# Kernel tuning notes

Measured on AMD Instinct MI355X. Metric: run time of the kernel, lower is better.

The kernel has to match this reference:

```python
import jax, jax.numpy as jnp
import numpy as np
from jax.ops import segment_sum, segment_max

N, E, F_IN, H1, H2, HEADS, OUT, G = 50000, 800000, 64, 64, 64, 4, 32, 500

def setup_inputs() -> dict:
    key = jax.random.key(0)
    ks = jax.random.split(key, 12)
    x = jax.random.normal(ks[0], (N, F_IN), dtype=jnp.float32)
    edge_index = jax.random.randint(ks[1], (2, E), 0, N, dtype=jnp.int64)
    batch = jnp.sort(jax.random.randint(ks[2], (N,), 0, G, dtype=jnp.int64))
    def glorot(k, shape):
        fan = shape[0] + shape[-1]
        return jax.random.uniform(k, shape, jnp.float32, -1.0, 1.0) * jnp.sqrt(6.0 / fan)
    return {
        "x": x,
        "edge_index": edge_index,
        "batch": batch,
        "gcn_W": glorot(ks[3], (F_IN, H1)),
        "gcn_b": jnp.zeros((H1,), jnp.float32),
        "gat_W": glorot(ks[4], (H1, HEADS * H2)),
        "att_src": glorot(ks[5], (HEADS, H2)),
        "att_dst": glorot(ks[6], (HEADS, H2)),
        "gat_b": jnp.zeros((HEADS * H2,), jnp.float32),
        "out_W": glorot(ks[7], (HEADS * H2, OUT)),
        "out_b": jnp.zeros((OUT,), jnp.float32),
    }

def reference(x, edge_index, batch, gcn_W, gcn_b, gat_W, att_src, att_dst, gat_b, out_W, out_b):
    n = x.shape[0]
    loop = jnp.arange(n)
    # edges with self-loops: src (j) -> dst (i), PyG convention
    src = jnp.concatenate([edge_index[0], loop])
    dst = jnp.concatenate([edge_index[1], loop])

    # ---- GCNConv: symmetric normalized scatter-add ----
    h = x @ gcn_W                                            # [N, H1]
    deg = segment_sum(jnp.ones_like(dst, dtype=h.dtype), dst, num_segments=n)
    dinv = jnp.where(deg > 0, jax.lax.rsqrt(deg), 0.0)       # deg^{-1/2}
    norm = dinv[src] * dinv[dst]                             # [E']
    h = segment_sum(norm[:, None] * h[src], dst, num_segments=n) + gcn_b
    h = jax.nn.relu(h)

    # ---- GATConv: per-edge attention + segment softmax over dst ----
    g = (h @ gat_W).reshape(n, HEADS, H2)                    # [N, H, C]
    a_s = jnp.einsum('nhc,hc->nh', g, att_src)               # [N, H]
    a_d = jnp.einsum('nhc,hc->nh', g, att_dst)
    e = jax.nn.leaky_relu(a_s[src] + a_d[dst], 0.2)          # [E', H]
    m = segment_max(e, dst, num_segments=n)                  # every node has a self-loop
    e = jnp.exp(e - m[dst])
    denom = segment_sum(e, dst, num_segments=n)
    alpha = e / denom[dst]                                   # [E', H]
    agg = segment_sum(alpha[:, :, None] * g[src], dst, num_segments=n)  # [N, H, C]
    z = jax.nn.relu(agg.reshape(n, HEADS * H2) + gat_b)

    # ---- global mean pool over graphs + output linear ----
    cnt = segment_sum(jnp.ones((n,), z.dtype), batch, num_segments=G)
    pooled = segment_sum(z, batch, num_segments=G) / jnp.maximum(cnt, 1.0)[:, None]
    return pooled @ out_W + out_b
```

## Files before the change

### kernel.cpp

```cpp
#include <hip/hip_runtime.h>
#include <math.h>

#define NN 50000
#define NE 800000
#define NEP (NE + NN)
#define NGRAPH 500
#define NOUT 32
#define NBLK 196

typedef _Float16 half4 __attribute__((ext_vector_type(4)));
typedef _Float16 half2v __attribute__((ext_vector_type(2)));

__device__ __forceinline__ float lrelu(float x) { return x > 0.f ? x : 0.2f * x; }
__device__ __forceinline__ half2v bch2(float f) { return __builtin_bit_cast(half2v, f); }

__device__ __forceinline__ unsigned fkey(float f) {
    unsigned b = __float_as_uint(f);
    return (b & 0x80000000u) ? ~b : (b | 0x80000000u);
}
__device__ __forceinline__ float funkey(unsigned k) {
    unsigned b = (k & 0x80000000u) ? (k & 0x7fffffffu) : ~k;
    return __uint_as_float(b);
}


__global__ void k_count(const int* __restrict__ dst, int* __restrict__ cnt,
                        int* __restrict__ pos) {
    int e = blockIdx.x * blockDim.x + threadIdx.x;
    if (e < NE) pos[e] = atomicAdd(&cnt[dst[e]], 1);
}

__global__ __launch_bounds__(256) void k_scan1(const int* __restrict__ cnt, int* __restrict__ bsum,
                                               float* __restrict__ pool, float* __restrict__ cnt_g) {
    __shared__ int buf[256];
    int gid = blockIdx.x * 256 + threadIdx.x;
    int v = (gid < NN) ? (cnt[gid] + 1) : 0;
    buf[threadIdx.x] = v;
    for (int j = gid; j < NGRAPH * 256; j += NBLK * 256) pool[j] = 0.f;
    if (gid < NGRAPH) cnt_g[gid] = 0.f;
    __syncthreads();
    for (int off = 128; off; off >>= 1) {
        if (threadIdx.x < off) buf[threadIdx.x] += buf[threadIdx.x + off];
        __syncthreads();
    }
    if (threadIdx.x == 0) bsum[blockIdx.x] = buf[0];
}

__global__ __launch_bounds__(256) void k_scan3(const int* __restrict__ cnt,
                                               const int* __restrict__ bsum,
                                               int* __restrict__ row_ptr,
                                               float* __restrict__ dinv,
                                               int* __restrict__ col) {
    __shared__ int sb[256];
    __shared__ int buf[256];
    int tid = threadIdx.x;
    int bv = (tid < NBLK) ? bsum[tid] : 0;
    sb[tid] = bv;
    __syncthreads();
    for (int off = 1; off < 256; off <<= 1) {
        int t = (tid >= off) ? sb[tid - off] : 0;
        __syncthreads();
        sb[tid] += t;
        __syncthreads();
    }
    int blockoff = (blockIdx.x == 0) ? 0 : sb[blockIdx.x - 1];
    int i = blockIdx.x * 256 + tid;
    int v = (i < NN) ? (cnt[i] + 1) : 0;
    buf[tid] = v;
    __syncthreads();
    for (int off = 1; off < 256; off <<= 1) {
        int t = (tid >= off) ? buf[tid - off] : 0;
        __syncthreads();
        buf[tid] += t;
        __syncthreads();
    }
    if (i < NN) {
        int rp = blockoff + buf[tid] - v;
        row_ptr[i] = rp;
        dinv[i] = rsqrtf((float)(cnt[i] + 1));
        col[rp] = i;
    }
    if (i == 0) row_ptr[NN] = NEP;
}

__global__ void k_fill(const int* __restrict__ src, const int* __restrict__ dst,
                       const int* __restrict__ row_ptr, const int* __restrict__ pos,
                       int* __restrict__ col) {
    int idx = blockIdx.x * blockDim.x + threadIdx.x;
    if (idx < NE) {
        int d = dst[idx];
        col[row_ptr[d] + 1 + pos[idx]] = src[idx];
    }
}


__global__ __launch_bounds__(256) void k_gemm64(const float* __restrict__ A,
                                                const float* __restrict__ B,
                                                const float* __restrict__ dinv,
                                                _Float16* __restrict__ C16, int n) {
    __shared__ float Bs[64 * 64];
    __shared__ float As[64 * 68];
    int tid = threadIdx.x;
    int rb = blockIdx.x * 64;
    for (int i = tid; i < 1024; i += 256) ((float4*)Bs)[i] = ((const float4*)B)[i];
    for (int i = tid; i < 1024; i += 256) {
        int r = i >> 4, c = i & 15;
        int row = rb + r; if (row >= n) row = n - 1;
        ((float4*)As)[r * 17 + c] = ((const float4*)A)[(size_t)row * 16 + c];
    }
    __syncthreads();
    int lane = tid & 63, wv = tid >> 6;
    int fl = lane & 15, sub = lane >> 4;
    int r0 = wv * 16 + sub * 4;
    const float4* Bs4 = (const float4*)Bs;
    float4 acc0 = {0,0,0,0}, acc1 = {0,0,0,0}, acc2 = {0,0,0,0}, acc3 = {0,0,0,0};
#pragma unroll 4
    for (int k = 0; k < 64; ++k) {
        float4 b4 = Bs4[k * 16 + fl];
        float a0 = As[(r0 + 0) * 68 + k];
        float a1 = As[(r0 + 1) * 68 + k];
        float a2 = As[(r0 + 2) * 68 + k];
        float a3 = As[(r0 + 3) * 68 + k];
        acc0.x += a0 * b4.x; acc0.y += a0 * b4.y; acc0.z += a0 * b4.z; acc0.w += a0 * b4.w;
        acc1.x += a1 * b4.x; acc1.y += a1 * b4.y; acc1.z += a1 * b4.z; acc1.w += a1 * b4.w;
        acc2.x += a2 * b4.x; acc2.y += a2 * b4.y; acc2.z += a2 * b4.z; acc2.w += a2 * b4.w;
        acc3.x += a3 * b4.x; acc3.y += a3 * b4.y; acc3.z += a3 * b4.z; acc3.w += a3 * b4.w;
    }
    int row = rb + r0;
    float d0 = dinv[row + 0 < n ? row + 0 : n - 1];
    float d1 = dinv[row + 1 < n ? row + 1 : n - 1];
    float d2 = dinv[row + 2 < n ? row + 2 : n - 1];
    float d3 = dinv[row + 3 < n ? row + 3 : n - 1];
    half4 h0, h1, h2, h3;
    h0.x=(_Float16)(acc0.x*d0); h0.y=(_Float16)(acc0.y*d0); h0.z=(_Float16)(acc0.z*d0); h0.w=(_Float16)(acc0.w*d0);
    h1.x=(_Float16)(acc1.x*d1); h1.y=(_Float16)(acc1.y*d1); h1.z=(_Float16)(acc1.z*d1); h1.w=(_Float16)(acc1.w*d1);
    h2.x=(_Float16)(acc2.x*d2); h2.y=(_Float16)(acc2.y*d2); h2.z=(_Float16)(acc2.z*d2); h2.w=(_Float16)(acc2.w*d2);
    h3.x=(_Float16)(acc3.x*d3); h3.y=(_Float16)(acc3.y*d3); h3.z=(_Float16)(acc3.z*d3); h3.w=(_Float16)(acc3.w*d3);
    if (row + 0 < n) ((half4*)(C16 + (size_t)(row + 0) * 64))[fl] = h0;
    if (row + 1 < n) ((half4*)(C16 + (size_t)(row + 1) * 64))[fl] = h1;
    if (row + 2 < n) ((half4*)(C16 + (size_t)(row + 2) * 64))[fl] = h2;
    if (row + 3 < n) ((half4*)(C16 + (size_t)(row + 3) * 64))[fl] = h3;
}


__global__ void k_uv(const float* __restrict__ gat_W, const float* __restrict__ att_src,
                     const float* __restrict__ att_dst, float* __restrict__ UV) {
    int idx = blockIdx.x * blockDim.x + threadIdx.x;
    if (idx >= 512) return;
    int f = idx >> 3, o = idx & 7, h = o & 3;
    const float* av = (o < 4) ? att_src : att_dst;
    float s = 0.f;
#pragma unroll 8
    for (int c = 0; c < 64; ++c) s += gat_W[f * 256 + h * 64 + c] * av[h * 64 + c];
    UV[idx] = s;
}


__global__ void k_w16t(const float* __restrict__ W, _Float16* __restrict__ W16T) {
    int idx = blockIdx.x * blockDim.x + threadIdx.x;
    if (idx >= 64 * 256) return;
    int c = idx >> 6, f = idx & 63;
    W16T[idx] = (_Float16)W[f * 256 + c];
}


__global__ __launch_bounds__(256) void k_gcn_agg(const _Float16* __restrict__ hxs16,
                                                 const int* __restrict__ row_ptr,
                                                 const int* __restrict__ col,
                                                 const float* __restrict__ dinv,
                                                 const float* __restrict__ bias,
                                                 const float* __restrict__ UV,
                                                 _Float16* __restrict__ h16,
                                                 float* __restrict__ a_s,
                                                 float* __restrict__ a_d) {
    int wid = (blockIdx.x * blockDim.x + threadIdx.x) >> 6;
    int lane = threadIdx.x & 63;
    if (wid >= NN) return;
    int slot = lane >> 4;
    int fl   = lane & 15;
    int s0 = row_ptr[wid], s1 = row_ptr[wid + 1];
    float di = dinv[wid];
    const half4* hx4 = (const half4*)hxs16;
    float ax = 0.f, ay = 0.f, az = 0.f, aw = 0.f;
    int k = s0 + slot;
    for (; k + 12 < s1; k += 16) {
        int i0 = col[k], i1 = col[k + 4], i2 = col[k + 8], i3 = col[k + 12];
        half4 v0 = hx4[(size_t)i0 * 16 + fl];
        half4 v1 = hx4[(size_t)i1 * 16 + fl];
        half4 v2 = hx4[(size_t)i2 * 16 + fl];
        half4 v3 = hx4[(size_t)i3 * 16 + fl];
        ax += ((float)v0.x + (float)v1.x) + ((float)v2.x + (float)v3.x);
        ay += ((float)v0.y + (float)v1.y) + ((float)v2.y + (float)v3.y);
        az += ((float)v0.z + (float)v1.z) + ((float)v2.z + (float)v3.z);
        aw += ((float)v0.w + (float)v1.w) + ((float)v2.w + (float)v3.w);
    }
    for (; k < s1; k += 4) {
        half4 v = hx4[(size_t)col[k] * 16 + fl];
        ax += (float)v.x; ay += (float)v.y;
        az += (float)v.z; aw += (float)v.w;
    }
    ax += __shfl_xor(ax, 16); ax += __shfl_xor(ax, 32);
    ay += __shfl_xor(ay, 16); ay += __shfl_xor(ay, 32);
    az += __shfl_xor(az, 16); az += __shfl_xor(az, 32);
    aw += __shfl_xor(aw, 16); aw += __shfl_xor(aw, 32);
    float4 bb = ((const float4*)bias)[fl];
    float zx = fmaxf(ax * di + bb.x, 0.f);
    float zy = fmaxf(ay * di + bb.y, 0.f);
    float zz = fmaxf(az * di + bb.z, 0.f);
    float zw = fmaxf(aw * di + bb.w, 0.f);
    if (slot == 0) {
        half4 z;
        z.x = (_Float16)zx; z.y = (_Float16)zy; z.z = (_Float16)zz; z.w = (_Float16)zw;
        ((half4*)(h16 + (size_t)wid * 64))[fl] = z;
    }
    int f0 = fl * 4;
    float ps = zx * UV[(f0 + 0) * 8 + slot] + zy * UV[(f0 + 1) * 8 + slot]
             + zz * UV[(f0 + 2) * 8 + slot] + zw * UV[(f0 + 3) * 8 + slot];
    float pd = zx * UV[(f0 + 0) * 8 + 4 + slot] + zy * UV[(f0 + 1) * 8 + 4 + slot]
             + zz * UV[(f0 + 2) * 8 + 4 + slot] + zw * UV[(f0 + 3) * 8 + 4 + slot];
    ps += __shfl_xor(ps, 1); pd += __shfl_xor(pd, 1);
    ps += __shfl_xor(ps, 2); pd += __shfl_xor(pd, 2);
    ps += __shfl_xor(ps, 4); pd += __shfl_xor(pd, 4);
    ps += __shfl_xor(ps, 8); pd += __shfl_xor(pd, 8);
    if (fl == 0) {
        a_s[wid * 4 + slot] = ps;
        a_d[wid * 4 + slot] = pd;
    }
}


__global__ __launch_bounds__(256) void k_gmax(const float* __restrict__ a_s,
                                              unsigned* __restrict__ gmaxU) {
    __shared__ unsigned sm[4];
    int tid = threadIdx.x;
    if (tid < 4) sm[tid] = 0u;
    __syncthreads();
    float mx = -1e30f, my = -1e30f, mz = -1e30f, mw = -1e30f;
    int stride = gridDim.x * 256;
    for (int n = blockIdx.x * 256 + tid; n < NN; n += stride) {
        float4 v = ((const float4*)a_s)[n];
        mx = fmaxf(mx, v.x); my = fmaxf(my, v.y);
        mz = fmaxf(mz, v.z); mw = fmaxf(mw, v.w);
    }
    atomicMax(&sm[0], fkey(mx)); atomicMax(&sm[1], fkey(my));
    atomicMax(&sm[2], fkey(mz)); atomicMax(&sm[3], fkey(mw));
    __syncthreads();
    if (tid < 4) atomicMax(&gmaxU[tid], sm[tid]);
}


__global__ __launch_bounds__(256) void k_gat_h(const _Float16* __restrict__ h16,
                                               const float* __restrict__ a_s,
                                               const float* __restrict__ a_d,
                                               const int* __restrict__ row_ptr,
                                               const int* __restrict__ col,
                                               const unsigned* __restrict__ gmaxU,
                                               _Float16* __restrict__ aggH) {
    int tid = threadIdx.x;
    int wv = tid >> 6, lane = tid & 63;
    int wid = blockIdx.x * 4 + wv;
    int slot = lane >> 4;
    int fl = lane & 15;

    int s0 = row_ptr[wid], s1 = row_ptr[wid + 1];
    float4 ad4 = ((const float4*)a_d)[wid];
    float M0 = lrelu(funkey(gmaxU[0]) + ad4.x);
    float M1 = lrelu(funkey(gmaxU[1]) + ad4.y);
    float M2 = lrelu(funkey(gmaxU[2]) + ad4.z);
    float M3 = lrelu(funkey(gmaxU[3]) + ad4.w);
    const half4* h4 = (const half4*)h16;
    const float4* as4 = (const float4*)a_s;

    float t0 = 1e-30f, t1 = 1e-30f, t2 = 1e-30f, t3 = 1e-30f;
    float4 A0 = {0,0,0,0}, A1 = {0,0,0,0}, A2 = {0,0,0,0}, A3 = {0,0,0,0};

    int k = s0 + slot;
    for (; k + 4 < s1; k += 8) {
        int ia = col[k], ib = col[k + 4];
        float4 ea = as4[ia];
        float4 eb = as4[ib];
        half4 va = h4[(size_t)ia * 16 + fl];
        half4 vb = h4[(size_t)ib * 16 + fl];
        float wa0 = __expf(lrelu(ea.x + ad4.x) - M0);
        float wa1 = __expf(lrelu(ea.y + ad4.y) - M1);
        float wa2 = __expf(lrelu(ea.z + ad4.z) - M2);
        float wa3 = __expf(lrelu(ea.w + ad4.w) - M3);
        float wb0 = __expf(lrelu(eb.x + ad4.x) - M0);
        float wb1 = __expf(lrelu(eb.y + ad4.y) - M1);
        float wb2 = __expf(lrelu(eb.z + ad4.z) - M2);
        float wb3 = __expf(lrelu(eb.w + ad4.w) - M3);
        t0 += wa0 + wb0; t1 += wa1 + wb1; t2 += wa2 + wb2; t3 += wa3 + wb3;
        float vax = (float)va.x, vay = (float)va.y, vaz = (float)va.z, vaw = (float)va.w;
        float vbx = (float)vb.x, vby = (float)vb.y, vbz = (float)vb.z, vbw = (float)vb.w;
        A0.x += wa0 * vax + wb0 * vbx; A0.y += wa0 * vay + wb0 * vby;
        A0.z += wa0 * vaz + wb0 * vbz; A0.w += wa0 * vaw + wb0 * vbw;
        A1.x += wa1 * vax + wb1 * vbx; A1.y += wa1 * vay + wb1 * vby;
        A1.z += wa1 * vaz + wb1 * vbz; A1.w += wa1 * vaw + wb1 * vbw;
        A2.x += wa2 * vax + wb2 * vbx; A2.y += wa2 * vay + wb2 * vby;
        A2.z += wa2 * vaz + wb2 * vbz; A2.w += wa2 * vaw + wb2 * vbw;
        A3.x += wa3 * vax + wb3 * vbx; A3.y += wa3 * vay + wb3 * vby;
        A3.z += wa3 * vaz + wb3 * vbz; A3.w += wa3 * vaw + wb3 * vbw;
    }
    if (k < s1) {
        int ia = col[k];
        float4 ea = as4[ia];
        half4 va = h4[(size_t)ia * 16 + fl];
        float wa0 = __expf(lrelu(ea.x + ad4.x) - M0);
        float wa1 = __expf(lrelu(ea.y + ad4.y) - M1);
        float wa2 = __expf(lrelu(ea.z + ad4.z) - M2);
        float wa3 = __expf(lrelu(ea.w + ad4.w) - M3);
        t0 += wa0; t1 += wa1; t2 += wa2; t3 += wa3;
        float vax = (float)va.x, vay = (float)va.y, vaz = (float)va.z, vaw = (float)va.w;
        A0.x += wa0 * vax; A0.y += wa0 * vay; A0.z += wa0 * vaz; A0.w += wa0 * vaw;
        A1.x += wa1 * vax; A1.y += wa1 * vay; A1.z += wa1 * vaz; A1.w += wa1 * vaw;
        A2.x += wa2 * vax; A2.y += wa2 * vay; A2.z += wa2 * vaz; A2.w += wa2 * vaw;
        A3.x += wa3 * vax; A3.y += wa3 * vay; A3.z += wa3 * vaz; A3.w += wa3 * vaw;
    }
#define REDX(x) x += __shfl_xor(x, 16); x += __shfl_xor(x, 32);
    REDX(t0) REDX(t1) REDX(t2) REDX(t3)
    REDX(A0.x) REDX(A0.y) REDX(A0.z) REDX(A0.w)
    REDX(A1.x) REDX(A1.y) REDX(A1.z) REDX(A1.w)
    REDX(A2.x) REDX(A2.y) REDX(A2.z) REDX(A2.w)
    REDX(A3.x) REDX(A3.y) REDX(A3.z) REDX(A3.w)
#undef REDX
    float rsel = slot == 0 ? t0 : slot == 1 ? t1 : slot == 2 ? t2 : t3;
    float4 Asel = slot == 0 ? A0 : slot == 1 ? A1 : slot == 2 ? A2 : A3;
    float r = 1.f / rsel;
    half4 o;
    o.x = (_Float16)(Asel.x * r); o.y = (_Float16)(Asel.y * r);
    o.z = (_Float16)(Asel.z * r); o.w = (_Float16)(Asel.w * r);
    ((half4*)(aggH + (size_t)wid * 256))[lane] = o;
}


__global__ __launch_bounds__(256) void k_post2(const _Float16* __restrict__ aggH,
                                               const _Float16* __restrict__ W16T,
                                               const float* __restrict__ gat_b,
                                               const int* __restrict__ batch,
                                               float* __restrict__ pool,
                                               float* __restrict__ cnt_g) {
    int tid = threadIdx.x;
    int lane = tid & 63;
    int wv = __builtin_amdgcn_readfirstlane(tid >> 6);
    int h = blockIdx.y;
    int c = h * 64 + lane;
    const float4* wp = (const float4*)(W16T + (size_t)c * 64);
    float4 Wb[8];
#pragma unroll
    for (int i = 0; i < 8; ++i) Wb[i] = wp[i];
    float gb = gat_b[c];

    int rbeg = (blockIdx.x * 4 + wv) * 32;
    int rend = rbeg + 32; if (rend > NN) rend = NN;

    float psum = 0.f;
    int curb = -1, rcnt = 0;
#pragma unroll 2
    for (int row = rbeg; row < rend; ++row) {
        int b = batch[row];
        if (b != curb) {
            if (curb >= 0) {
                atomicAdd(&pool[(size_t)curb * 256 + c], psum);
                if (h == 0 && lane == 0) atomicAdd(&cnt_g[curb], (float)rcnt);
            }
            psum = 0.f; rcnt = 0; curb = b;
        }
        const float4* ap = (const float4*)(aggH + (size_t)row * 256 + h * 64);
        float4 Ab[8];
#pragma unroll
        for (int i = 0; i < 8; ++i) Ab[i] = ap[i];
        float ac0 = 0.f, ac1 = 0.f, ac2 = 0.f, ac3 = 0.f;
#pragma unroll
        for (int i = 0; i < 8; ++i) {
            ac0 = __builtin_amdgcn_fdot2(bch2(Ab[i].x), bch2(Wb[i].x), ac0, false);
            ac1 = __builtin_amdgcn_fdot2(bch2(Ab[i].y), bch2(Wb[i].y), ac1, false);
            ac2 = __builtin_amdgcn_fdot2(bch2(Ab[i].z), bch2(Wb[i].z), ac2, false);
            ac3 = __builtin_amdgcn_fdot2(bch2(Ab[i].w), bch2(Wb[i].w), ac3, false);
        }
        float acc = (ac0 + ac1) + (ac2 + ac3);
        psum += fmaxf(acc + gb, 0.f);
        ++rcnt;
    }
    if (curb >= 0) {
        atomicAdd(&pool[(size_t)curb * 256 + c], psum);
        if (h == 0 && lane == 0) atomicAdd(&cnt_g[curb], (float)rcnt);
    }
}


__global__ void k_out(const float* __restrict__ pool, const float* __restrict__ cnt_g,
                      const float* __restrict__ W, const float* __restrict__ b,
                      float* __restrict__ out) {
    int idx = blockIdx.x * blockDim.x + threadIdx.x;
    if (idx >= NGRAPH * NOUT) return;
    int gg = idx >> 5, o = idx & 31;
    float c = cnt_g[gg];
    c = c > 1.f ? c : 1.f;
    float rinv = 1.f / c;
    const float* p = pool + (size_t)gg * 256;
    float acc = 0.f;
#pragma unroll 8
    for (int f = 0; f < 256; ++f) acc += p[f] * W[f * 32 + o];
    out[idx] = acc * rinv + b[o];
}


extern "C" void kernel_launch(void* const* d_in, const int* in_sizes, int n_in,
                              void* d_out, int out_size, void* d_ws, size_t ws_size,
                              hipStream_t stream) {
    const float* x       = (const float*)d_in[0];
    const int*   eidx    = (const int*)d_in[1];
    const int*   batch   = (const int*)d_in[2];
    const float* gcn_W   = (const float*)d_in[3];
    const float* gcn_b   = (const float*)d_in[4];
    const float* gat_W   = (const float*)d_in[5];
    const float* att_src = (const float*)d_in[6];
    const float* att_dst = (const float*)d_in[7];
    const float* gat_b   = (const float*)d_in[8];
    const float* out_W   = (const float*)d_in[9];
    const float* out_b   = (const float*)d_in[10];
    float* out = (float*)d_out;

    const int* src = eidx;
    const int* dst = eidx + NE;

    size_t off = 0;
    auto carve = [&](size_t bytes) -> char* {
        char* p = (char*)d_ws + off;
        off += (bytes + 255) & ~(size_t)255;
        return p;
    };
    int*      cnt     = (int*)carve(NN * sizeof(int));
    int*      pos     = (int*)carve((size_t)NE * sizeof(int));
    int*      row_ptr = (int*)carve((NN + 1) * sizeof(int));
    int*      bsum    = (int*)carve(256 * sizeof(int));
    int*      colb    = (int*)carve((size_t)NEP * sizeof(int));
    float*    dinv    = (float*)carve(NN * sizeof(float));
    _Float16* hx16    = (_Float16*)carve((size_t)NN * 64 * sizeof(_Float16));
    _Float16* h16     = (_Float16*)carve((size_t)NN * 64 * sizeof(_Float16));
    _Float16* aggH16  = (_Float16*)carve((size_t)NN * 256 * sizeof(_Float16));
    float*    a_s     = (float*)carve((size_t)NN * 4 * sizeof(float));
    float*    a_d     = (float*)carve((size_t)NN * 4 * sizeof(float));
    float*    UV      = (float*)carve(64 * 8 * sizeof(float));
    _Float16* W16T    = (_Float16*)carve(64 * 256 * sizeof(_Float16));
    unsigned* gmaxU   = (unsigned*)carve(4 * sizeof(unsigned));
    float*    pool    = (float*)carve((size_t)NGRAPH * 256 * sizeof(float));
    float*    cnt_g   = (float*)carve(NGRAPH * sizeof(float));

    hipMemsetAsync(cnt, 0, NN * sizeof(int), stream);
    hipMemsetAsync(gmaxU, 0, 4 * sizeof(unsigned), stream);

    k_count<<<(NE + 255) / 256, 256, 0, stream>>>(dst, cnt, pos);
    k_scan1<<<NBLK, 256, 0, stream>>>(cnt, bsum, pool, cnt_g);
    k_scan3<<<NBLK, 256, 0, stream>>>(cnt, bsum, row_ptr, dinv, colb);
    k_fill<<<(NE + 255) / 256, 256, 0, stream>>>(src, dst, row_ptr, pos, colb);

    k_uv<<<2, 256, 0, stream>>>(gat_W, att_src, att_dst, UV);
    k_w16t<<<64, 256, 0, stream>>>(gat_W, W16T);

    k_gemm64<<<(NN + 63) / 64, 256, 0, stream>>>(x, gcn_W, dinv, hx16, NN);
    k_gcn_agg<<<(NN * 64 + 255) / 256, 256, 0, stream>>>(hx16, row_ptr, colb, dinv, gcn_b,
                                                         UV, h16, a_s, a_d);

    k_gmax<<<128, 256, 0, stream>>>(a_s, gmaxU);
    k_gat_h<<<NN / 4, 256, 0, stream>>>(h16, a_s, a_d, row_ptr, colb, gmaxU, aggH16);

    k_post2<<<dim3(391, 4), 256, 0, stream>>>(aggH16, W16T, gat_b, batch, pool, cnt_g);

    k_out<<<(NGRAPH * NOUT + 255) / 256, 256, 0, stream>>>(pool, cnt_g, out_W, out_b, out);
}
```

Before: 317.5 us.

## Fuse small setup kernels, fold global max into GCN aggregation, add nontemporal accesses

Merges the UV and transposed-W16 setup kernels into a single launch, replaces the memset of gmaxU with zeroing inside the scan kernel, and computes the per-head global max of a_s inside the GCN aggregation kernel via shared and global atomics, dropping the separate k_gmax pass. Many streaming loads and stores (col indices, intermediate features, attention logits) become nontemporal to reduce cache pollution. The GEMM inner loop is rewritten with vector-type arithmetic. The goal is fewer launches and less cache thrashing, at the cost of extra atomics per block and the risk that nontemporal hints hurt reused data such as col, which is read by both aggregation kernels.

```diff
diff --git a/kernel.cpp b/kernel.cpp
--- a/kernel.cpp
+++ b/kernel.cpp
@@ -10,6 +10,7 @@
 
 typedef _Float16 half4 __attribute__((ext_vector_type(4)));
 typedef _Float16 half2v __attribute__((ext_vector_type(2)));
+typedef float f4v __attribute__((ext_vector_type(4)));
 
 __device__ __forceinline__ float lrelu(float x) { return x > 0.f ? x : 0.2f * x; }
 __device__ __forceinline__ half2v bch2(float f) { return __builtin_bit_cast(half2v, f); }
@@ -27,17 +28,22 @@
 __global__ void k_count(const int* __restrict__ dst, int* __restrict__ cnt,
                         int* __restrict__ pos) {
     int e = blockIdx.x * blockDim.x + threadIdx.x;
-    if (e < NE) pos[e] = atomicAdd(&cnt[dst[e]], 1);
+    if (e < NE) {
+        int p = atomicAdd(&cnt[dst[e]], 1);
+        __builtin_nontemporal_store(p, pos + e);
+    }
 }
 
 __global__ __launch_bounds__(256) void k_scan1(const int* __restrict__ cnt, int* __restrict__ bsum,
-                                               float* __restrict__ pool, float* __restrict__ cnt_g) {
+                                               float* __restrict__ pool, float* __restrict__ cnt_g,
+                                               unsigned* __restrict__ gmaxU) {
     __shared__ int buf[256];
     int gid = blockIdx.x * 256 + threadIdx.x;
     int v = (gid < NN) ? (cnt[gid] + 1) : 0;
     buf[threadIdx.x] = v;
     for (int j = gid; j < NGRAPH * 256; j += NBLK * 256) pool[j] = 0.f;
     if (gid < NGRAPH) cnt_g[gid] = 0.f;
+    if (gid < 4) gmaxU[gid] = 0u;
     __syncthreads();
     for (int off = 128; off; off >>= 1) {
         if (threadIdx.x < off) buf[threadIdx.x] += buf[threadIdx.x + off];
@@ -89,7 +95,7 @@
     int idx = blockIdx.x * blockDim.x + threadIdx.x;
     if (idx < NE) {
         int d = dst[idx];
-        col[row_ptr[d] + 1 + pos[idx]] = src[idx];
+        __builtin_nontemporal_store(src[idx], col + row_ptr[d] + 1 + pos[idx]);
     }
 }
 
@@ -102,29 +108,30 @@
     __shared__ float As[64 * 68];
     int tid = threadIdx.x;
     int rb = blockIdx.x * 64;
-    for (int i = tid; i < 1024; i += 256) ((float4*)Bs)[i] = ((const float4*)B)[i];
+    for (int i = tid; i < 1024; i += 256) ((f4v*)Bs)[i] = ((const f4v*)B)[i];
     for (int i = tid; i < 1024; i += 256) {
         int r = i >> 4, c = i & 15;
         int row = rb + r; if (row >= n) row = n - 1;
-        ((float4*)As)[r * 17 + c] = ((const float4*)A)[(size_t)row * 16 + c];
+        f4v t = __builtin_nontemporal_load((const f4v*)A + (size_t)row * 16 + c);
+        ((f4v*)As)[r * 17 + c] = t;
     }
     __syncthreads();
     int lane = tid & 63, wv = tid >> 6;
     int fl = lane & 15, sub = lane >> 4;
     int r0 = wv * 16 + sub * 4;
-    const float4* Bs4 = (const float4*)Bs;
-    float4 acc0 = {0,0,0,0}, acc1 = {0,0,0,0}, acc2 = {0,0,0,0}, acc3 = {0,0,0,0};
+    const f4v* Bs4 = (const f4v*)Bs;
+    f4v acc0 = {0,0,0,0}, acc1 = {0,0,0,0}, acc2 = {0,0,0,0}, acc3 = {0,0,0,0};
 #pragma unroll 4
     for (int k = 0; k < 64; ++k) {
-        float4 b4 = Bs4[k * 16 + fl];
+        f4v b4 = Bs4[k * 16 + fl];
         float a0 = As[(r0 + 0) * 68 + k];
         float a1 = As[(r0 + 1) * 68 + k];
         float a2 = As[(r0 + 2) * 68 + k];
         float a3 = As[(r0 + 3) * 68 + k];
-        acc0.x += a0 * b4.x; acc0.y += a0 * b4.y; acc0.z += a0 * b4.z; acc0.w += a0 * b4.w;
-        acc1.x += a1 * b4.x; acc1.y += a1 * b4.y; acc1.z += a1 * b4.z; acc1.w += a1 * b4.w;
-        acc2.x += a2 * b4.x; acc2.y += a2 * b4.y; acc2.z += a2 * b4.z; acc2.w += a2 * b4.w;
-        acc3.x += a3 * b4.x; acc3.y += a3 * b4.y; acc3.z += a3 * b4.z; acc3.w += a3 * b4.w;
+        acc0 += a0 * b4;
+        acc1 += a1 * b4;
+        acc2 += a2 * b4;
+        acc3 += a3 * b4;
     }
     int row = rb + r0;
     float d0 = dinv[row + 0 < n ? row + 0 : n - 1];
@@ -143,24 +150,22 @@
 }
 
 
-__global__ void k_uv(const float* __restrict__ gat_W, const float* __restrict__ att_src,
-                     const float* __restrict__ att_dst, float* __restrict__ UV) {
+__global__ void k_uvw(const float* __restrict__ gat_W, const float* __restrict__ att_src,
+                      const float* __restrict__ att_dst, float* __restrict__ UV,
+                      _Float16* __restrict__ W16T) {
     int idx = blockIdx.x * blockDim.x + threadIdx.x;
-    if (idx >= 512) return;
-    int f = idx >> 3, o = idx & 7, h = o & 3;
-    const float* av = (o < 4) ? att_src : att_dst;
-    float s = 0.f;
+    if (idx < 64 * 256) {
+        int c = idx >> 6, f = idx & 63;
+        W16T[idx] = (_Float16)gat_W[f * 256 + c];
+    }
+    if (idx < 512) {
+        int f = idx >> 3, o = idx & 7, h = o & 3;
+        const float* av = (o < 4) ? att_src : att_dst;
+        float s = 0.f;
 #pragma unroll 8
-    for (int c = 0; c < 64; ++c) s += gat_W[f * 256 + h * 64 + c] * av[h * 64 + c];
-    UV[idx] = s;
-}
-
-
-__global__ void k_w16t(const float* __restrict__ W, _Float16* __restrict__ W16T) {
-    int idx = blockIdx.x * blockDim.x + threadIdx.x;
-    if (idx >= 64 * 256) return;
-    int c = idx >> 6, f = idx & 63;
-    W16T[idx] = (_Float16)W[f * 256 + c];
+        for (int c = 0; c < 64; ++c) s += gat_W[f * 256 + h * 64 + c] * av[h * 64 + c];
+        UV[idx] = s;
+    }
 }
 
 
@@ -172,10 +177,14 @@
                                                  const float* __restrict__ UV,
                                                  _Float16* __restrict__ h16,
                                                  float* __restrict__ a_s,
-                                                 float* __restrict__ a_d) {
-    int wid = (blockIdx.x * blockDim.x + threadIdx.x) >> 6;
-    int lane = threadIdx.x & 63;
-    if (wid >= NN) return;
+                                                 float* __restrict__ a_d,
+                                                 unsigned* __restrict__ gmaxU) {
+    __shared__ unsigned smax[4];
+    int tid = threadIdx.x;
+    if (tid < 4) smax[tid] = 0u;
+    __syncthreads();
+    int wid = (blockIdx.x * blockDim.x + tid) >> 6;
+    int lane = tid & 63;
     int slot = lane >> 4;
     int fl   = lane & 15;
     int s0 = row_ptr[wid], s1 = row_ptr[wid + 1];
@@ -184,7 +193,10 @@
     float ax = 0.f, ay = 0.f, az = 0.f, aw = 0.f;
     int k = s0 + slot;
     for (; k + 12 < s1; k += 16) {
-        int i0 = col[k], i1 = col[k + 4], i2 = col[k + 8], i3 = col[k + 12];
+        int i0 = __builtin_nontemporal_load(col + k);
+        int i1 = __builtin_nontemporal_load(col + k + 4);
+        int i2 = __builtin_nontemporal_load(col + k + 8);
+        int i3 = __builtin_nontemporal_load(col + k + 12);
         half4 v0 = hx4[(size_t)i0 * 16 + fl];
         half4 v1 = hx4[(size_t)i1 * 16 + fl];
         half4 v2 = hx4[(size_t)i2 * 16 + fl];
@@ -195,7 +207,8 @@
         aw += ((float)v0.w + (float)v1.w) + ((float)v2.w + (float)v3.w);
     }
     for (; k < s1; k += 4) {
-        half4 v = hx4[(size_t)col[k] * 16 + fl];
+        int i0 = __builtin_nontemporal_load(col + k);
+        half4 v = hx4[(size_t)i0 * 16 + fl];
         ax += (float)v.x; ay += (float)v.y;
         az += (float)v.z; aw += (float)v.w;
     }
@@ -211,7 +224,7 @@
     if (slot == 0) {
         half4 z;
         z.x = (_Float16)zx; z.y = (_Float16)zy; z.z = (_Float16)zz; z.w = (_Float16)zw;
-        ((half4*)(h16 + (size_t)wid * 64))[fl] = z;
+        __builtin_nontemporal_store(z, (half4*)(h16 + (size_t)wid * 64) + fl);
     }
     int f0 = fl * 4;
     float ps = zx * UV[(f0 + 0) * 8 + slot] + zy * UV[(f0 + 1) * 8 + slot]
@@ -223,29 +236,12 @@
     ps += __shfl_xor(ps, 4); pd += __shfl_xor(pd, 4);
     ps += __shfl_xor(ps, 8); pd += __shfl_xor(pd, 8);
     if (fl == 0) {
-        a_s[wid * 4 + slot] = ps;
-        a_d[wid * 4 + slot] = pd;
-    }
-}
-
-
-__global__ __launch_bounds__(256) void k_gmax(const float* __restrict__ a_s,
-                                              unsigned* __restrict__ gmaxU) {
-    __shared__ unsigned sm[4];
-    int tid = threadIdx.x;
-    if (tid < 4) sm[tid] = 0u;
-    __syncthreads();
-    float mx = -1e30f, my = -1e30f, mz = -1e30f, mw = -1e30f;
-    int stride = gridDim.x * 256;
-    for (int n = blockIdx.x * 256 + tid; n < NN; n += stride) {
-        float4 v = ((const float4*)a_s)[n];
-        mx = fmaxf(mx, v.x); my = fmaxf(my, v.y);
-        mz = fmaxf(mz, v.z); mw = fmaxf(mw, v.w);
-    }
-    atomicMax(&sm[0], fkey(mx)); atomicMax(&sm[1], fkey(my));
-    atomicMax(&sm[2], fkey(mz)); atomicMax(&sm[3], fkey(mw));
-    __syncthreads();
-    if (tid < 4) atomicMax(&gmaxU[tid], sm[tid]);
+        __builtin_nontemporal_store(ps, a_s + wid * 4 + slot);
+        __builtin_nontemporal_store(pd, a_d + wid * 4 + slot);
+        atomicMax(&smax[slot], fkey(ps));
+    }
+    __syncthreads();
+    if (tid < 4) atomicMax(&gmaxU[tid], smax[tid]);
 }
 
 
@@ -276,7 +272,8 @@
 
     int k = s0 + slot;
     for (; k + 4 < s1; k += 8) {
-        int ia = col[k], ib = col[k + 4];
+        int ia = __builtin_nontemporal_load(col + k);
+        int ib = __builtin_nontemporal_load(col + k + 4);
         float4 ea = as4[ia];
         float4 eb = as4[ib];
         half4 va = h4[(size_t)ia * 16 + fl];
@@ -302,7 +299,7 @@
         A3.z += wa3 * vaz + wb3 * vbz; A3.w += wa3 * vaw + wb3 * vbw;
     }
     if (k < s1) {
-        int ia = col[k];
+        int ia = __builtin_nontemporal_load(col + k);
         float4 ea = as4[ia];
         half4 va = h4[(size_t)ia * 16 + fl];
         float wa0 = __expf(lrelu(ea.x + ad4.x) - M0);
@@ -329,7 +326,7 @@
     half4 o;
     o.x = (_Float16)(Asel.x * r); o.y = (_Float16)(Asel.y * r);
     o.z = (_Float16)(Asel.z * r); o.w = (_Float16)(Asel.w * r);
-    ((half4*)(aggH + (size_t)wid * 256))[lane] = o;
+    __builtin_nontemporal_store(o, (half4*)(aggH + (size_t)wid * 256) + lane);
 }
 
 
@@ -344,8 +341,8 @@
     int wv = __builtin_amdgcn_readfirstlane(tid >> 6);
     int h = blockIdx.y;
     int c = h * 64 + lane;
-    const float4* wp = (const float4*)(W16T + (size_t)c * 64);
-    float4 Wb[8];
+    const f4v* wp = (const f4v*)(W16T + (size_t)c * 64);
+    f4v Wb[8];
 #pragma unroll
     for (int i = 0; i < 8; ++i) Wb[i] = wp[i];
     float gb = gat_b[c];
@@ -365,10 +362,10 @@
             }
             psum = 0.f; rcnt = 0; curb = b;
         }
-        const float4* ap = (const float4*)(aggH + (size_t)row * 256 + h * 64);
-        float4 Ab[8];
+        const f4v* ap = (const f4v*)(aggH + (size_t)row * 256 + h * 64);
+        f4v Ab[8];
 #pragma unroll
-        for (int i = 0; i < 8; ++i) Ab[i] = ap[i];
+        for (int i = 0; i < 8; ++i) Ab[i] = __builtin_nontemporal_load(ap + i);
         float ac0 = 0.f, ac1 = 0.f, ac2 = 0.f, ac3 = 0.f;
 #pragma unroll
         for (int i = 0; i < 8; ++i) {
@@ -448,21 +445,18 @@
     float*    cnt_g   = (float*)carve(NGRAPH * sizeof(float));
 
     hipMemsetAsync(cnt, 0, NN * sizeof(int), stream);
-    hipMemsetAsync(gmaxU, 0, 4 * sizeof(unsigned), stream);
 
     k_count<<<(NE + 255) / 256, 256, 0, stream>>>(dst, cnt, pos);
-    k_scan1<<<NBLK, 256, 0, stream>>>(cnt, bsum, pool, cnt_g);
+    k_scan1<<<NBLK, 256, 0, stream>>>(cnt, bsum, pool, cnt_g, gmaxU);
     k_scan3<<<NBLK, 256, 0, stream>>>(cnt, bsum, row_ptr, dinv, colb);
     k_fill<<<(NE + 255) / 256, 256, 0, stream>>>(src, dst, row_ptr, pos, colb);
 
-    k_uv<<<2, 256, 0, stream>>>(gat_W, att_src, att_dst, UV);
-    k_w16t<<<64, 256, 0, stream>>>(gat_W, W16T);
+    k_uvw<<<64, 256, 0, stream>>>(gat_W, att_src, att_dst, UV, W16T);
 
     k_gemm64<<<(NN + 63) / 64, 256, 0, stream>>>(x, gcn_W, dinv, hx16, NN);
     k_gcn_agg<<<(NN * 64 + 255) / 256, 256, 0, stream>>>(hx16, row_ptr, colb, dinv, gcn_b,
-                                                         UV, h16, a_s, a_d);
-
-    k_gmax<<<128, 256, 0, stream>>>(a_s, gmaxU);
+                                                         UV, h16, a_s, a_d, gmaxU);
+
     k_gat_h<<<NN / 4, 256, 0, stream>>>(h16, a_s, a_d, row_ptr, colb, gmaxU, aggH16);
 
     k_post2<<<dim3(391, 4), 256, 0, stream>>>(aggH16, W16T, gat_b, batch, pool, cnt_g);
```

Result: slower. 419.7 us (+32.2%).
